# Kernel optimization log

Measured on AMD Instinct MI355X. Metric: run time of the kernel, lower is better.

## Reference

```python
import jax, jax.numpy as jnp
import numpy as np

OUT_FEATURES = 4096
IN_FEATURES = 16384
NNZ = 2_000_000
BATCH = 128


def setup_inputs() -> dict:
    key = jax.random.key(0)
    k1, k2, k3, k4, k5 = jax.random.split(key, 5)
    inputs = jax.random.normal(k1, (BATCH, IN_FEATURES), dtype=jnp.float32)
    # learned sparse weight values and bias (uniform init like reset_parameters)
    bound = 1.0 / (IN_FEATURES ** 0.5)
    values = jax.random.uniform(k2, (NNZ,), minval=-bound, maxval=bound, dtype=jnp.float32)
    bias = jax.random.uniform(k3, (OUT_FEATURES,), minval=-bound, maxval=bound, dtype=jnp.float32)
    # fixed COO connectivity: rows -> out_features, cols -> in_features
    rows = jax.random.randint(k4, (NNZ,), 0, OUT_FEATURES, dtype=jnp.int32)
    cols = jax.random.randint(k5, (NNZ,), 0, IN_FEATURES, dtype=jnp.int32)
    return {"inputs": inputs, "values": values, "bias": bias, "rows": rows, "cols": cols}


def reference(inputs, values, bias, rows, cols):
    # out[b, r] = sum_{k: rows[k]==r} values[k] * inputs[b, cols[k]]  (+ bias[r])
    # Gather input columns per nnz entry, scale, then scatter-add into output rows.
    contrib = inputs[:, cols] * values            # [B, nnz]
    out = jax.ops.segment_sum(contrib.T, rows, num_segments=OUT_FEATURES).T  # [B, out_features]
    return out + bias
```

## Files before the change

kernel.cpp:

```cpp
#include <hip/hip_runtime.h>
#include <hip/hip_fp16.h>

#define NNZ    2000000
#define BATCH  128
#define IN_F   16384
#define OUT_F  4096
#define NCH    1024
#define CHUNK  1956
#define NBK    1024
#define RPB    4
#define BK_CAP 2240

__device__ inline int mbcnt64(unsigned long long m) {
  return __builtin_amdgcn_mbcnt_hi((unsigned)(m >> 32),
         __builtin_amdgcn_mbcnt_lo((unsigned)m, 0));
}

__global__ __launch_bounds__(512)
void k_localsort(const int* __restrict__ rows, const int* __restrict__ cols,
                 const float* __restrict__ vals, int* __restrict__ desc,
                 int2* __restrict__ pairs) {
  __shared__ int  lrows[CHUNK];
  __shared__ int2 stage[CHUNK];
  __shared__ int  h[NBK], cur[NBK];
  __shared__ int  wsums[8];
  const int t = threadIdx.x, c = blockIdx.x;
  const int lane = t & 63, w = t >> 6;
  const int base = c * CHUNK;
  const int n = min(CHUNK, NNZ - base);
  const int n4 = n >> 2;

  h[t] = 0; h[t + 512] = 0;
  __syncthreads();
  for (int i = t; i < n4; i += 512) {
    const int4 r4 = ((const int4*)(rows + base))[i];
    ((int4*)lrows)[i] = r4;
    atomicAdd(&h[r4.x >> 2], 1);
    atomicAdd(&h[r4.y >> 2], 1);
    atomicAdd(&h[r4.z >> 2], 1);
    atomicAdd(&h[r4.w >> 2], 1);
  }
  __syncthreads();
  const int v0 = h[2 * t], v1 = h[2 * t + 1];
  const int sv = v0 + v1;
  int x = sv;
#pragma unroll
  for (int off = 1; off < 64; off <<= 1) { int y = __shfl_up(x, off); if (lane >= off) x += y; }
  if (lane == 63) wsums[w] = x;
  __syncthreads();
  int wex = 0;
#pragma unroll
  for (int j = 0; j < 8; ++j) { const int sj = wsums[j]; wex += (j < w) ? sj : 0; }
  const int excl = wex + x - sv;
  cur[2 * t] = excl;
  cur[2 * t + 1] = excl + v0;
  ((int2*)desc)[c * 512 + t] = make_int2((excl << 8) | v0, ((excl + v0) << 8) | v1);
  __syncthreads();
  for (int i = t; i < n4; i += 512) {
    const int4   r4 = ((const int4*)lrows)[i];
    const int4   c4 = ((const int4*)(cols + base))[i];
    const float4 f4 = ((const float4*)(vals + base))[i];
    int pos;
    pos = atomicAdd(&cur[r4.x >> 2], 1); stage[pos] = make_int2((r4.x << 14) | c4.x, __float_as_int(f4.x));
    pos = atomicAdd(&cur[r4.y >> 2], 1); stage[pos] = make_int2((r4.y << 14) | c4.y, __float_as_int(f4.y));
    pos = atomicAdd(&cur[r4.z >> 2], 1); stage[pos] = make_int2((r4.z << 14) | c4.z, __float_as_int(f4.z));
    pos = atomicAdd(&cur[r4.w >> 2], 1); stage[pos] = make_int2((r4.w << 14) | c4.w, __float_as_int(f4.w));
  }
  __syncthreads();
  const int nh = n >> 1;
  for (int j = t; j < nh; j += 512)
    ((int4*)(pairs + base))[j] = ((const int4*)stage)[j];
}

__global__ __launch_bounds__(512)
void k_cscan(const int* __restrict__ desc, unsigned* __restrict__ rdesc,
             int* __restrict__ btot) {
  __shared__ int tile[8 * 1025];
  const int t = threadIdx.x, blk = blockIdx.x;
  const int b0 = blk * 8;
  const int lane = t & 63, w = t >> 6;
#pragma unroll
  for (int it = 0; it < 16; ++it) {
    const int cc = it * 64 + (t >> 3);
    tile[(t & 7) * 1025 + cc] = desc[cc * NBK + b0 + (t & 7)];
  }
  __syncthreads();
  int carry = 0;
#pragma unroll
  for (int j = 0; j < 16; ++j) {
    const int cc = j * 64 + lane;
    const unsigned d = (unsigned)tile[w * 1025 + cc];
    const int len = (int)(d & 255u);
    int x = len;
#pragma unroll
    for (int off = 1; off < 64; off <<= 1) { int y = __shfl_up(x, off); if (lane >= off) x += y; }
    const int ex = carry + x - len;
    rdesc[(b0 + w) * NCH + cc] = (d << 12) | (unsigned)ex;
    carry += __shfl(x, 63);
  }
  if (lane == 0) btot[b0 + w] = carry;
}

__global__ __launch_bounds__(256)
void k_transpose(const float* __restrict__ in, __half* __restrict__ inT) {
  __shared__ float tile[32][33];
  const int tx = threadIdx.x, ty = threadIdx.y;
  const int c0 = blockIdx.x * 32, b0 = blockIdx.y * 32;
#pragma unroll
  for (int j = 0; j < 32; j += 8)
    tile[ty + j][tx] = in[(b0 + ty + j) * IN_F + c0 + tx];
  __syncthreads();
#pragma unroll
  for (int j = 0; j < 32; j += 8)
    inT[(size_t)(c0 + ty + j) * BATCH + b0 + tx] = __float2half(tile[tx][ty + j]);
}

#define REFILL(SL, KK) do { \
    const int idx = (hh_ + 2 * (KK)) * 8 + 2 * g; \
    const bool vld = idx < nr; \
    const int i0_ = vld ? (s + idx) : 0; \
    uint4 pp = *((const uint4*)(sorted + i0_)); \
    if (!vld) { pp.y = 0u; pp.w = 0u; } \
    x##SL##0 = inT[(pp.x & 16383u) * 16 + q]; \
    x##SL##1 = inT[(pp.z & 16383u) * 16 + q]; \
    pv##SL = make_uint2(pp.y, pp.w); \
  } while (0)

#define FMAH(SL) do { \
    const __half2 hv0 = __float2half2_rn(__uint_as_float(pv##SL.x)); \
    const __half2 hv1 = __float2half2_rn(__uint_as_float(pv##SL.y)); \
    const __half2* h0 = (const __half2*)&x##SL##0; \
    const __half2* h1 = (const __half2*)&x##SL##1; \
    hac0 = __hfma2(hv0, h0[0], hac0); hac1 = __hfma2(hv0, h0[1], hac1); \
    hac2 = __hfma2(hv0, h0[2], hac2); hac3 = __hfma2(hv0, h0[3], hac3); \
    hac0 = __hfma2(hv1, h1[0], hac0); hac1 = __hfma2(hv1, h1[1], hac1); \
    hac2 = __hfma2(hv1, h1[2], hac2); hac3 = __hfma2(hv1, h1[3], hac3); \
  } while (0)

#define STAGE(SL, NEXTKK) do { FMAH(SL); REFILL(SL, NEXTKK); } while (0)

#define FLUSH() do { \
    float2 f0 = __half22float2(hac0), f1 = __half22float2(hac1); \
    float2 f2 = __half22float2(hac2), f3 = __half22float2(hac3); \
    a0 += f0.x; a1 += f0.y; a2 += f1.x; a3 += f1.y; \
    a4 += f2.x; a5 += f2.y; a6 += f3.x; a7 += f3.y; \
    hac0 = hz; hac1 = hz; hac2 = hz; hac3 = hz; \
  } while (0)

__global__ __launch_bounds__(512, 8)
void k_spmm(const uint4* __restrict__ inT, const int2* __restrict__ pairs,
            const unsigned* __restrict__ rdesc, const int* __restrict__ btot,
            const float* __restrict__ bias, float* __restrict__ out) {
  __shared__ __align__(16) int2 staging[BK_CAP];
  __shared__ __align__(16) int2 sorted[BK_CAP + 8];
  __shared__ int  exd[NCH];
  __shared__ int  wrun[32];
  __shared__ unsigned long long wmask[32];
  __shared__ int  wcnt[32];
  __shared__ int  lst[RPB + 1];
  const int t = threadIdx.x, b = blockIdx.x;
  const int w = t >> 6, lane = t & 63;
  const int n = min(btot[b], BK_CAP);
  const int nrnd = (n + 511) & ~511;

  exd[t] = (int)rdesc[b * NCH + t];
  exd[t + 512] = (int)rdesc[b * NCH + t + 512];
  __syncthreads();
  for (int i = t; i < n; i += 512) {
    int lo = 0, hi = NCH - 1;
#pragma unroll
    for (int st = 0; st < 10; ++st) {
      const int mid = (lo + hi + 1) >> 1;
      if ((exd[mid] & 4095) <= i) lo = mid; else hi = mid - 1;
    }
    const unsigned d = (unsigned)exd[lo];
    staging[i] = pairs[lo * CHUNK + (int)(d >> 20) + (i - (int)(d & 4095u))];
  }
  __syncthreads();

  int cnt = 0;
  for (int i = w * 64 + lane; i < nrnd; i += 512) {
    const bool valid = i < n;
    const int key = valid ? staging[i].x : 0;
    const int r4 = valid ? ((key >> 14) & 3) : 4;
    unsigned long long m[4];
#pragma unroll
    for (int r = 0; r < 4; ++r) m[r] = __ballot(r4 == r);
    if (lane < 4) cnt += __popcll(m[lane]);
  }
  if (lane < 4) wcnt[w * 4 + lane] = cnt;
  __syncthreads();

  if (w == 0 && lane < 32) {
    const int v = wcnt[lane];
    int x = v;
#pragma unroll
    for (int off = 4; off < 32; off <<= 1) { int y = __shfl_up(x, off); if (lane >= off) x += y; }
    const int exw = x - v;
    int lstr = 0, tpad = 0;
#pragma unroll
    for (int rr = 0; rr < 4; ++rr) {
      const int tr = __shfl(x, 28 + rr);
      const int trE = (tr + 1) & ~1;
      if ((lane & 3) > rr) lstr += trE;
      tpad += trE;
    }
    wrun[lane] = lstr + exw;
    if (lane < 4) lst[lane] = lstr;
    if (lane == 0) lst[RPB] = tpad;
    if (lane >= 28) {
      if (x & 1) sorted[lstr + x] = make_int2(0, 0);
    }
  }
  __syncthreads();

  for (int i = w * 64 + lane; i < nrnd; i += 512) {
    const bool valid = i < n;
    const int2 p = valid ? staging[i] : make_int2(0, 0);
    const int r4 = valid ? ((p.x >> 14) & 3) : 4;
    unsigned long long m[4];
#pragma unroll
    for (int r = 0; r < 4; ++r) m[r] = __ballot(r4 == r);
    if (lane < 4) wmask[w * 4 + lane] = m[lane];
    if (valid) {
      const int rank = wrun[w * 4 + r4] + mbcnt64(wmask[w * 4 + r4]);
      sorted[rank] = p;
    }
    if (lane < 4) wrun[w * 4 + lane] += __popcll(m[lane]);
  }
  __syncthreads();

  const int rloc = w >> 1, hh_ = w & 1;
  const int r = b * RPB + rloc;
  const int g = lane >> 4, q = lane & 15;
  const int s = lst[rloc];
  const int nr = lst[rloc + 1] - s;
  const int nsteps = (nr + 7) >> 3;
  const int K = (nsteps + 1) >> 1;
  const int K3 = ((K + 2) / 3) * 3;

  float a0 = 0.f, a1 = 0.f, a2 = 0.f, a3 = 0.f, a4 = 0.f, a5 = 0.f, a6 = 0.f, a7 = 0.f;
  const __half2 hz = __float2half2_rn(0.f);
  __half2 hac0 = hz, hac1 = hz, hac2 = hz, hac3 = hz;
  uint4 xA0, xA1, xB0, xB1, xC0, xC1;
  uint2 pvA, pvB, pvC;

  REFILL(A, 0);
  REFILL(B, 1);
  REFILL(C, 2);
  for (int kk = 0; kk < K3; kk += 3) {
    STAGE(A, kk + 3);
    STAGE(B, kk + 4);
    STAGE(C, kk + 5);
    FLUSH();
  }

  a0 += __shfl_xor(a0, 16); a0 += __shfl_xor(a0, 32);
  a1 += __shfl_xor(a1, 16); a1 += __shfl_xor(a1, 32);
  a2 += __shfl_xor(a2, 16); a2 += __shfl_xor(a2, 32);
  a3 += __shfl_xor(a3, 16); a3 += __shfl_xor(a3, 32);
  a4 += __shfl_xor(a4, 16); a4 += __shfl_xor(a4, 32);
  a5 += __shfl_xor(a5, 16); a5 += __shfl_xor(a5, 32);
  a6 += __shfl_xor(a6, 16); a6 += __shfl_xor(a6, 32);
  a7 += __shfl_xor(a7, 16); a7 += __shfl_xor(a7, 32);

  float (*part)[BATCH] = (float (*)[BATCH])staging;
  if (hh_ == 1 && g == 0) {
    const int o = q * 8;
    part[rloc][o + 0] = a0; part[rloc][o + 1] = a1;
    part[rloc][o + 2] = a2; part[rloc][o + 3] = a3;
    part[rloc][o + 4] = a4; part[rloc][o + 5] = a5;
    part[rloc][o + 6] = a6; part[rloc][o + 7] = a7;
  }
  __syncthreads();
  if (hh_ == 0 && g == 0) {
    const float bs_ = bias[r];
    const int o = q * 8;
    out[(o + 0) * OUT_F + r] = a0 + part[rloc][o + 0] + bs_;
    out[(o + 1) * OUT_F + r] = a1 + part[rloc][o + 1] + bs_;
    out[(o + 2) * OUT_F + r] = a2 + part[rloc][o + 2] + bs_;
    out[(o + 3) * OUT_F + r] = a3 + part[rloc][o + 3] + bs_;
    out[(o + 4) * OUT_F + r] = a4 + part[rloc][o + 4] + bs_;
    out[(o + 5) * OUT_F + r] = a5 + part[rloc][o + 5] + bs_;
    out[(o + 6) * OUT_F + r] = a6 + part[rloc][o + 6] + bs_;
    out[(o + 7) * OUT_F + r] = a7 + part[rloc][o + 7] + bs_;
  }
}

extern "C" void kernel_launch(void* const* d_in, const int* in_sizes, int n_in,
                              void* d_out, int out_size, void* d_ws, size_t ws_size,
                              hipStream_t stream) {
  const float* inputs = (const float*)d_in[0];
  const float* values = (const float*)d_in[1];
  const float* bias   = (const float*)d_in[2];
  const int*   rows   = (const int*)d_in[3];
  const int*   cols   = (const int*)d_in[4];
  float* out = (float*)d_out;

  char* ws = (char*)d_ws;
  __half*   inputT = (__half*)(ws);
  int2*     pairs  = (int2*)(ws + 4194304);
  int*      desc   = (int*)(ws + 20217856);
  unsigned* rdesc  = (unsigned*)(ws + 24412160);
  int*      btot   = (int*)(ws + 28606464);

  k_localsort<<<NCH,     512, 0, stream>>>(rows, cols, values, desc, pairs);
  k_cscan    <<<NBK / 8, 512, 0, stream>>>(desc, rdesc, btot);
  k_transpose<<<dim3(IN_F / 32, BATCH / 32), dim3(32, 8), 0, stream>>>(inputs, inputT);
  k_spmm     <<<NBK,     512, 0, stream>>>((const uint4*)inputT, pairs, rdesc, btot, bias, out);
}
```

Baseline: 133.2 us.

## Split descriptor scan into separate transpose kernel and re-read rows from global

The column-scan kernel no longer gathers the strided descriptor matrix into shared memory. A new tiled transpose kernel now writes the descriptors in bucket-major order, and the scan reads them contiguously with smaller blocks and more of them. The scan writes its output in place over the transposed buffer. Separately, the local sort drops its shared-memory copy of row indices and reloads them from global memory in the second pass, which lowers LDS use and may raise occupancy. The cost is an extra kernel launch and a second global read of the rows.

```diff
diff --git a/kernel.cpp b/kernel.cpp
--- a/kernel.cpp
+++ b/kernel.cpp
@@ -20,7 +20,6 @@
 void k_localsort(const int* __restrict__ rows, const int* __restrict__ cols,
                  const float* __restrict__ vals, int* __restrict__ desc,
                  int2* __restrict__ pairs) {
-  __shared__ int  lrows[CHUNK];
   __shared__ int2 stage[CHUNK];
   __shared__ int  h[NBK], cur[NBK];
   __shared__ int  wsums[8];
@@ -34,7 +33,6 @@
   __syncthreads();
   for (int i = t; i < n4; i += 512) {
     const int4 r4 = ((const int4*)(rows + base))[i];
-    ((int4*)lrows)[i] = r4;
     atomicAdd(&h[r4.x >> 2], 1);
     atomicAdd(&h[r4.y >> 2], 1);
     atomicAdd(&h[r4.z >> 2], 1);
@@ -57,7 +55,7 @@
   ((int2*)desc)[c * 512 + t] = make_int2((excl << 8) | v0, ((excl + v0) << 8) | v1);
   __syncthreads();
   for (int i = t; i < n4; i += 512) {
-    const int4   r4 = ((const int4*)lrows)[i];
+    const int4   r4 = ((const int4*)(rows + base))[i];
     const int4   c4 = ((const int4*)(cols + base))[i];
     const float4 f4 = ((const float4*)(vals + base))[i];
     int pos;
@@ -72,33 +70,38 @@
     ((int4*)(pairs + base))[j] = ((const int4*)stage)[j];
 }
 
-__global__ __launch_bounds__(512)
-void k_cscan(const int* __restrict__ desc, unsigned* __restrict__ rdesc,
+__global__ __launch_bounds__(256)
+void k_dtr(const int* __restrict__ desc, int* __restrict__ descT) {
+  __shared__ int tile[32][33];
+  const int tx = threadIdx.x, ty = threadIdx.y;
+  const int x0 = blockIdx.x * 32, y0 = blockIdx.y * 32;
+#pragma unroll
+  for (int j = 0; j < 32; j += 8)
+    tile[ty + j][tx] = desc[(y0 + ty + j) * NBK + x0 + tx];
+  __syncthreads();
+#pragma unroll
+  for (int j = 0; j < 32; j += 8)
+    descT[(x0 + ty + j) * NCH + y0 + tx] = tile[tx][ty + j];
+}
+
+__global__ __launch_bounds__(256)
+void k_cscan(const int* __restrict__ descT, unsigned* __restrict__ rdesc,
              int* __restrict__ btot) {
-  __shared__ int tile[8 * 1025];
-  const int t = threadIdx.x, blk = blockIdx.x;
-  const int b0 = blk * 8;
-  const int lane = t & 63, w = t >> 6;
-#pragma unroll
-  for (int it = 0; it < 16; ++it) {
-    const int cc = it * 64 + (t >> 3);
-    tile[(t & 7) * 1025 + cc] = desc[cc * NBK + b0 + (t & 7)];
-  }
-  __syncthreads();
+  const int t = threadIdx.x, lane = t & 63, w = t >> 6;
+  const int b = blockIdx.x * 4 + w;
   int carry = 0;
 #pragma unroll
   for (int j = 0; j < 16; ++j) {
     const int cc = j * 64 + lane;
-    const unsigned d = (unsigned)tile[w * 1025 + cc];
+    const unsigned d = (unsigned)descT[b * NCH + cc];
     const int len = (int)(d & 255u);
     int x = len;
 #pragma unroll
     for (int off = 1; off < 64; off <<= 1) { int y = __shfl_up(x, off); if (lane >= off) x += y; }
-    const int ex = carry + x - len;
-    rdesc[(b0 + w) * NCH + cc] = (d << 12) | (unsigned)ex;
+    rdesc[b * NCH + cc] = (d << 12) | (unsigned)(carry + x - len);
     carry += __shfl(x, 63);
   }
-  if (lane == 0) btot[b0 + w] = carry;
+  if (lane == 0) btot[b] = carry;
 }
 
 __global__ __launch_bounds__(256)
@@ -301,11 +304,13 @@
   __half*   inputT = (__half*)(ws);
   int2*     pairs  = (int2*)(ws + 4194304);
   int*      desc   = (int*)(ws + 20217856);
-  unsigned* rdesc  = (unsigned*)(ws + 24412160);
+  int*      descT  = (int*)(ws + 24412160);
+  unsigned* rdesc  = (unsigned*)descT;
   int*      btot   = (int*)(ws + 28606464);
 
   k_localsort<<<NCH,     512, 0, stream>>>(rows, cols, values, desc, pairs);
-  k_cscan    <<<NBK / 8, 512, 0, stream>>>(desc, rdesc, btot);
+  k_dtr      <<<dim3(NBK / 32, NCH / 32), dim3(32, 8), 0, stream>>>(desc, descT);
+  k_cscan    <<<NBK / 4, 256, 0, stream>>>(descT, rdesc, btot);
   k_transpose<<<dim3(IN_F / 32, BATCH / 32), dim3(32, 8), 0, stream>>>(inputs, inputT);
   k_spmm     <<<NBK,     512, 0, stream>>>((const uint4*)inputT, pairs, rdesc, btot, bias, out);
 }
```

Result: no change. 133.9 us (+0.5%).
